# Kernel tuning notes

Measured on AMD Instinct MI355X. Metric: run time of the kernel, lower is better.

Reference implementation:

```python
import jax, jax.numpy as jnp
import numpy as np
from jax import lax

V, E, H, B, S = 100000, 256, 256, 16, 64
NEG = -1e9


def setup_inputs() -> dict:
    key = jax.random.key(0)
    ks = jax.random.split(key, 20)
    sc = 0.05
    inp = {
        "x": jax.random.randint(ks[0], (B, S), 0, V),
        "mask": jax.random.randint(ks[1], (B, S), 0, 2).astype(jnp.int32),
        "TASK": 0,
        # embedding table (pretrained embedding copied into nn.Embedding)
        "embed": jax.random.normal(ks[2], (V, E), jnp.float32) * sc,
        # shared LSTM (torch gate order i,f,g,o)
        "W_ih": jax.random.normal(ks[3], (4 * H, E), jnp.float32) * sc,
        "W_hh": jax.random.normal(ks[4], (4 * H, H), jnp.float32) * sc,
        "b_ih": jax.random.normal(ks[5], (4 * H,), jnp.float32) * sc,
        "b_hh": jax.random.normal(ks[6], (4 * H,), jnp.float32) * sc,
        # task-specific attention: Ws: (E+2H)->H, Us: H->1
        "Ws_w": jax.random.normal(ks[7], (H, E + 2 * H), jnp.float32) * sc,
        "Ws_b": jax.random.normal(ks[8], (H,), jnp.float32) * sc,
        "Us_w": jax.random.normal(ks[9], (1, H), jnp.float32) * sc,
        "Us_b": jax.random.normal(ks[10], (1,), jnp.float32) * sc,
        # message LSTM cell: gates from x_t, h_{t-1}, message Rt
        "Wx": jax.random.normal(ks[11], (4 * H, E), jnp.float32) * sc,
        "Wh": jax.random.normal(ks[12], (4 * H, H), jnp.float32) * sc,
        "Wm": jax.random.normal(ks[13], (4 * H, H), jnp.float32) * sc,
        "b_cell": jax.random.normal(ks[14], (4 * H,), jnp.float32) * sc,
        # final classifier
        "fc_w": jax.random.normal(ks[15], (1, H), jnp.float32) * sc,
        "fc_b": jax.random.normal(ks[16], (1,), jnp.float32) * sc,
    }
    return inp


def _lstm_gates(g, c):
    i, f, gg, o = jnp.split(g, 4, axis=-1)
    c_new = jax.nn.sigmoid(f) * c + jax.nn.sigmoid(i) * jnp.tanh(gg)
    h_new = jax.nn.sigmoid(o) * jnp.tanh(c_new)
    return h_new, c_new


def _forward(x, mask, embed, W_ih, W_hh, b_ih, b_hh, Ws_w, Ws_b, Us_w, Us_b,
             Wx, Wh, Wm, b_cell, fc_w, fc_b):
    b, s = x.shape
    h_dim = W_hh.shape[1]
    emb = embed[x]                              # [B,S,E]
    emb_t = jnp.transpose(emb, (1, 0, 2))       # [S,B,E]
    z = jnp.zeros((b, h_dim), emb.dtype)

    def shared_step(carry, e_t):
        h, c = carry
        g = e_t @ W_ih.T + h @ W_hh.T + (b_ih + b_hh)
        h, c = _lstm_gates(g, c)
        return (h, c), h

    _, shared_t = lax.scan(shared_step, (z, z), emb_t)   # [S,B,H]
    shared = jnp.transpose(shared_t, (1, 0, 2))          # [B,S,H]
    valid = mask != 0                                    # [B,S]

    def task_step(carry, e_t):
        h, c = carry
        h_task = jnp.broadcast_to(h[:, None, :], shared.shape)      # [B,S,H]
        cat = jnp.concatenate([shared, h_task, emb], axis=2)        # [B,S,E+2H]
        var2 = jnp.tanh(cat @ Ws_w.T + Ws_b)                        # [B,S,H]
        Si = (var2 @ Us_w.T + Us_b)[..., 0]                         # [B,S]
        att = jax.nn.softmax(jnp.where(valid, Si, NEG), axis=1)     # masked softmax over S
        Rt = jnp.einsum('bs,bsh->bh', att, shared)                  # [B,H]
        g = e_t @ Wx.T + h @ Wh.T + Rt @ Wm.T + b_cell
        h, c = _lstm_gates(g, c)
        return (h, c), None

    (h_last, _), _ = lax.scan(jax.checkpoint(task_step), (z, z), emb_t)
    return jax.nn.sigmoid(h_last @ fc_w.T + fc_b)        # [B,1]


def reference(x, mask, TASK, embed, W_ih, W_hh, b_ih, b_hh, Ws_w, Ws_b,
              Us_w, Us_b, Wx, Wh, Wm, b_cell, fc_w, fc_b):
    # TASK selects an entry of task_specific_lstm_list, but the list holds the
    # same module object num_tasks times, so one parameter set is used.
    del TASK
    return _forward(x, mask, embed, W_ih, W_hh, b_ih, b_hh, Ws_w, Ws_b,
                    Us_w, Us_b, Wx, Wh, Wm, b_cell, fc_w, fc_b)
```

## Files before the change

### kernel.cpp

```cpp
#include <hip/hip_runtime.h>

#define NEGV -1e9f

#define OFF_X1   0u
#define OFF_XX   1048576u
#define OFF_A    2097152u
#define OFF_SH   2359296u
#define OFF_SWM  2621440u
#define OFF_HX2  3670016u
#define OFF_HX4  3686400u
#define OFF_PSI  3702784u
#define OFF_AT   OFF_X1

__device__ __forceinline__ float sigf(float x) { return 1.f / (1.f + __expf(-x)); }
__device__ __forceinline__ float tanhfast(float x) {
  float e = __expf(2.f * x);
  return 1.f - __fdividef(2.f, e + 1.f);
}

__device__ __forceinline__ unsigned long long gloadU64(const unsigned long long* p) {
  return __hip_atomic_load(p, __ATOMIC_RELAXED, __HIP_MEMORY_SCOPE_AGENT);
}
__device__ __forceinline__ void gstoreU64(unsigned long long* p, unsigned long long v) {
  __hip_atomic_store(p, v, __ATOMIC_RELAXED, __HIP_MEMORY_SCOPE_AGENT);
}

__device__ __forceinline__ void tile_mm(const float* __restrict__ W, int ldw, int wcol0,
                                        int j0, const float* eL, float* wL, float acc[8]) {
  const int i = threadIdx.x >> 4, jj = threadIdx.x & 15;
  for (int kc = 0; kc < 4; ++kc) {
    __syncthreads();
    const int k0 = kc * 64;
    #pragma unroll
    for (int m = 0; m < 32; ++m) {
      int v = threadIdx.x + (m << 8);
      int row = v >> 6, col = v & 63;
      wL[row * 68 + col] = W[(j0 + row) * ldw + wcol0 + k0 + col];
    }
    __syncthreads();
    const float* ebase = eL + i * 260 + k0;
    #pragma unroll 4
    for (int k4 = 0; k4 < 16; ++k4) {
      float4 e4 = *(const float4*)(ebase + k4 * 4);
      #pragma unroll
      for (int u = 0; u < 8; ++u) {
        float4 w4 = *(const float4*)(wL + (jj + (u << 4)) * 68 + k4 * 4);
        acc[u] += e4.x * w4.x + e4.y * w4.y + e4.z * w4.z + e4.w * w4.w;
      }
    }
  }
}

__global__ __launch_bounds__(256) void k1_precompute(
    const int* __restrict__ x, const float* __restrict__ embed,
    const float* __restrict__ W_ih, const float* __restrict__ b_ih,
    const float* __restrict__ b_hh, const float* __restrict__ Ws_w,
    const float* __restrict__ Ws_b, const float* __restrict__ Wx,
    const float* __restrict__ b_cell, float* __restrict__ ws) {
  __shared__ float eL[16 * 260];
  __shared__ float wL[128 * 68];
  const int rt = blockIdx.x / 18, jb = blockIdx.x % 18;
  if (blockIdx.x == 0) {
    for (int i = threadIdx.x; i < 65536; i += 256) ws[OFF_HX2 + i] = 0.f;
  }
  for (int i = 0; i < 16; ++i) {
    int xi = x[rt * 16 + i];
    eL[i * 260 + threadIdx.x] = embed[xi * 256 + threadIdx.x];
  }
  const float* W; const float* bias1; const float* bias2 = nullptr;
  int ldw, wcol0, j0, ostride; float* out;
  if (jb < 8)       { W = W_ih; ldw = 256; wcol0 = 0;   j0 = jb * 128;        out = ws + OFF_X1; ostride = 1024; bias1 = b_ih; bias2 = b_hh; }
  else if (jb < 16) { W = Wx;   ldw = 256; wcol0 = 0;   j0 = (jb - 8) * 128;  out = ws + OFF_XX; ostride = 1024; bias1 = b_cell; }
  else              { W = Ws_w; ldw = 768; wcol0 = 512; j0 = (jb - 16) * 128; out = ws + OFF_A;  ostride = 256;  bias1 = Ws_b; }
  float acc[8];
  #pragma unroll
  for (int u = 0; u < 8; ++u) acc[u] = 0.f;
  tile_mm(W, ldw, wcol0, j0, eL, wL, acc);
  const int i = threadIdx.x >> 4, jj = threadIdx.x & 15;
  const int r = rt * 16 + i;
  #pragma unroll
  for (int u = 0; u < 8; ++u) {
    int j = j0 + jj + (u << 4);
    float bv = bias1[j] + (bias2 ? bias2[j] : 0.f);
    out[r * ostride + j] = acc[u] + bv;
  }
}

__global__ __launch_bounds__(512) void k2_shared_lstm(
    const float* __restrict__ W_hh, float* __restrict__ ws) {
  const int b = blockIdx.x & 15, j = blockIdx.x >> 4;
  const int t = threadIdx.x;
  const int rl = t >> 2, q = t & 3;
  const int grow = ((rl >> 5) << 8) + (j << 5) + (rl & 31);
  __shared__ float x1L[64 * 128];
  __shared__ __align__(16) float hL[256];
  __shared__ float gA[128];
  unsigned long long* hx = (unsigned long long*)(ws + OFF_HX2);
  float* sh = ws + OFF_SH;
  const float* X1 = ws + OFF_X1;

  float4 wv[16];
  {
    const float* wp = W_hh + grow * 256 + (q << 6);
    #pragma unroll
    for (int m = 0; m < 16; ++m) wv[m] = *(const float4*)(wp + 4 * m);
  }
  for (int v = t; v < 8192; v += 512) {
    int st = v >> 7, r = v & 127;
    int col = ((r >> 5) << 8) + (j << 5) + (r & 31);
    x1L[v] = X1[(b * 64 + st) * 1024 + col];
  }
  float c_reg = 0.f;
  __syncthreads();

  for (int st = 0; st < 64; ++st) {
    if (t < 256) {
      const unsigned long long* p = hx + (unsigned)(st & 1) * 4096u + b * 256 + t;
      unsigned long long v = gloadU64(p);
      while ((unsigned)(v >> 32) < (unsigned)st) v = gloadU64(p);
      hL[t] = __uint_as_float((unsigned)v);
    }
    __syncthreads();
    float p = 0.f;
    const float* hp = hL + (q << 6);
    #pragma unroll
    for (int m = 0; m < 16; ++m) {
      float4 h4 = *(const float4*)(hp + 4 * m);
      p += wv[m].x * h4.x + wv[m].y * h4.y + wv[m].z * h4.z + wv[m].w * h4.w;
    }
    p += __shfl_xor(p, 1); p += __shfl_xor(p, 2);
    if (q == 0) gA[rl] = p + x1L[st * 128 + rl];
    __syncthreads();
    if (t < 32) {
      float gi = gA[t], gf = gA[32 + t], gg = gA[64 + t], go = gA[96 + t];
      c_reg = sigf(gf) * c_reg + sigf(gi) * tanhfast(gg);
      float hn = sigf(go) * tanhfast(c_reg);
      sh[(b * 64 + st) * 256 + (j << 5) + t] = hn;
      unsigned long long pv = ((unsigned long long)(unsigned)(st + 1) << 32)
                            | (unsigned long long)__float_as_uint(hn);
      gstoreU64(hx + (unsigned)((st + 1) & 1) * 4096u + b * 256 + (j << 5) + t, pv);
    }
  }
}

__global__ __launch_bounds__(256) void k3_precompute2(
    const float* __restrict__ Ws_w, const float* __restrict__ Wm,
    float* __restrict__ ws) {
  __shared__ float eL[16 * 260];
  __shared__ float wL[128 * 68];
  const int rt = blockIdx.x / 10, jb = blockIdx.x % 10;
  const float* sh = ws + OFF_SH;
  for (int i = 0; i < 16; ++i)
    eL[i * 260 + threadIdx.x] = sh[(rt * 16 + i) * 256 + threadIdx.x];
  const float* W; int ldw, wcol0, j0; bool addmode;
  if (jb < 8) { W = Wm;   ldw = 256; wcol0 = 0; j0 = jb * 128;       addmode = false; }
  else        { W = Ws_w; ldw = 768; wcol0 = 0; j0 = (jb - 8) * 128; addmode = true; }
  float acc[8];
  #pragma unroll
  for (int u = 0; u < 8; ++u) acc[u] = 0.f;
  tile_mm(W, ldw, wcol0, j0, eL, wL, acc);
  const int i = threadIdx.x >> 4, jj = threadIdx.x & 15;
  const int r = rt * 16 + i;
  if (addmode) {
    const float* Aemb = ws + OFF_A;
    float* AT = ws + OFF_AT;
    const int bb = r >> 6, s = r & 63;
    #pragma unroll
    for (int u = 0; u < 8; ++u) {
      int j = j0 + jj + (u << 4);
      AT[bb * 16384 + j * 64 + s] = Aemb[r * 256 + j] + acc[u];
    }
  } else {
    float* out = ws + OFF_SWM;
    #pragma unroll
    for (int u = 0; u < 8; ++u) {
      int j = j0 + jj + (u << 4);
      out[r * 1024 + j] = acc[u];
    }
  }
}

__global__ __launch_bounds__(512) void k4_task_lstm(
    const int* __restrict__ mask, const float* __restrict__ Ws_w,
    const float* __restrict__ Us_w, const float* __restrict__ Wh,
    const float* __restrict__ fc_w, const float* __restrict__ fc_b,
    float* __restrict__ ws, float* __restrict__ out) {
  const int b = blockIdx.x & 15, j = blockIdx.x >> 4;
  const int t = threadIdx.x;
  const int rl = t >> 2, q = t & 3;
  const int grow = ((rl >> 5) << 8) + (j << 5) + (rl & 31);
  const int hwrow = t >> 4, hwc = t & 15;
  const int kq = t >> 6, sl = t & 63;

  __shared__ __align__(16) float swmB[4 * 128 * 20];
  __shared__ __align__(16) float aTo[32 * 65];
  __shared__ __align__(16) float hL[256];
  __shared__ float hwOwn[32];
  __shared__ float usOwn[32];
  __shared__ float part[8 * 64];
  __shared__ float psiA[512];
  __shared__ __align__(16) float attL[64];
  __shared__ float gA[128];
  __shared__ float redL[4];
  __shared__ int   mL[64];

  unsigned long long* hx   = (unsigned long long*)(ws + OFF_HX4);
  unsigned long long* psiX = (unsigned long long*)(ws + OFF_PSI);
  const float* AT  = ws + OFF_AT;
  const float* SWM = ws + OFF_SWM;
  const float* Xx  = ws + OFF_XX;

  float4 w2v[4];
  {
    const float* p2 = Ws_w + (j * 32 + hwrow) * 768 + 256 + (hwc << 4);
    #pragma unroll
    for (int m = 0; m < 4; ++m) w2v[m] = *(const float4*)(p2 + 4 * m);
  }
  float4 whv[16];
  {
    const float* pw = Wh + grow * 256 + (q << 6);
    #pragma unroll
    for (int m = 0; m < 16; ++m) whv[m] = *(const float4*)(pw + 4 * m);
  }
  for (int v = t; v < 2048; v += 512)
    aTo[(v >> 6) * 65 + (v & 63)] = AT[b * 16384 + j * 2048 + v];
  for (int v = t; v < 8192; v += 512) {
    int s = v >> 7, r = v & 127;
    int col = ((r >> 5) << 8) + (j << 5) + (r & 31);
    swmB[(s >> 4) * 2560 + r * 20 + (s & 15)] = SWM[(b * 64 + s) * 1024 + col];
  }
  if (t < 32) usOwn[t] = Us_w[j * 32 + t];
  if (t < 64) mL[t] = mask[b * 64 + t];
  float c_reg = 0.f;
  __syncthreads();

  for (int st = 0; st < 64; ++st) {
    float xx_r = 0.f;
    if (q == 0) xx_r = Xx[(b * 64 + st) * 1024 + grow];
    if (t < 256) {
      const unsigned long long* p = hx + (unsigned)(st & 1) * 4096u + b * 256 + t;
      unsigned long long v = gloadU64(p);
      while ((unsigned)(v >> 32) < (unsigned)st) v = gloadU64(p);
      hL[t] = __uint_as_float((unsigned)v);
    }
    __syncthreads();
    {
      const float* hp = hL + (hwc << 4);
      float p = 0.f;
      #pragma unroll
      for (int m = 0; m < 4; ++m) {
        float4 h4 = *(const float4*)(hp + 4 * m);
        p += w2v[m].x * h4.x + w2v[m].y * h4.y + w2v[m].z * h4.z + w2v[m].w * h4.w;
      }
      p += __shfl_xor(p, 1); p += __shfl_xor(p, 2);
      p += __shfl_xor(p, 4); p += __shfl_xor(p, 8);
      if (hwc == 0) hwOwn[hwrow] = p;
    }
    __syncthreads();
    {
      float ps = 0.f;
      #pragma unroll
      for (int i2 = 0; i2 < 4; ++i2) {
        int kk = (kq << 2) + i2;
        ps += usOwn[kk] * tanhfast(aTo[kk * 65 + sl] + hwOwn[kk]);
      }
      part[(kq << 6) + sl] = ps;
    }
    __syncthreads();
    if (t < 64) {
      float ps = 0.f;
      #pragma unroll
      for (int w = 0; w < 8; ++w) ps += part[(w << 6) + t];
      unsigned long long pv = ((unsigned long long)(unsigned)(st + 1) << 32)
                            | (unsigned long long)__float_as_uint(ps);
      gstoreU64(psiX + ((unsigned)(st & 1) * 16u + b) * 512u + (j << 6) + t, pv);
    }
    float pwh = 0.f;
    {
      const float* hp = hL + (q << 6);
      #pragma unroll
      for (int m = 0; m < 16; ++m) {
        float4 h4 = *(const float4*)(hp + 4 * m);
        pwh += whv[m].x * h4.x + whv[m].y * h4.y + whv[m].z * h4.z + whv[m].w * h4.w;
      }
    }
    {
      const unsigned long long* p = psiX + ((unsigned)(st & 1) * 16u + b) * 512u + t;
      unsigned long long v = gloadU64(p);
      while ((unsigned)(v >> 32) < (unsigned)(st + 1)) v = gloadU64(p);
      psiA[t] = __uint_as_float((unsigned)v);
    }
    __syncthreads();
    if (t < 64) {
      float acc = 0.f;
      #pragma unroll
      for (int w = 0; w < 8; ++w) acc += psiA[(w << 6) + t];
      float v = mL[t] ? acc : NEGV;
      float mx = v;
      #pragma unroll
      for (int d = 1; d < 64; d <<= 1) mx = fmaxf(mx, __shfl_xor(mx, d));
      float e = __expf(v - mx);
      float ssum = e;
      #pragma unroll
      for (int d = 1; d < 64; d <<= 1) ssum += __shfl_xor(ssum, d);
      attL[t] = e / ssum;
    }
    __syncthreads();
    {
      float p = pwh;
      const float* sb = swmB + q * 2560 + rl * 20;
      const float* atb = attL + (q << 4);
      #pragma unroll
      for (int i2 = 0; i2 < 4; ++i2) {
        float4 s4 = *(const float4*)(sb + 4 * i2);
        float4 a4 = *(const float4*)(atb + 4 * i2);
        p += s4.x * a4.x + s4.y * a4.y + s4.z * a4.z + s4.w * a4.w;
      }
      p += __shfl_xor(p, 1); p += __shfl_xor(p, 2);
      if (q == 0) gA[rl] = p + xx_r;
    }
    __syncthreads();
    if (t < 32) {
      float gi = gA[t], gf = gA[32 + t], gg = gA[64 + t], go = gA[96 + t];
      c_reg = sigf(gf) * c_reg + sigf(gi) * tanhfast(gg);
      float hn = sigf(go) * tanhfast(c_reg);
      unsigned long long pv = ((unsigned long long)(unsigned)(st + 1) << 32)
                            | (unsigned long long)__float_as_uint(hn);
      gstoreU64(hx + (unsigned)((st + 1) & 1) * 4096u + b * 256 + (j << 5) + t, pv);
    }
  }

  if (j == 0) {
    float v = 0.f;
    if (t < 256) {
      const unsigned long long* p = hx + 0 * 4096u + b * 256 + t;
      unsigned long long vv = gloadU64(p);
      while ((unsigned)(vv >> 32) < 64u) vv = gloadU64(p);
      v = __uint_as_float((unsigned)vv) * fc_w[t];
    }
    #pragma unroll
    for (int d = 1; d < 64; d <<= 1) v += __shfl_xor(v, d);
    if (t < 256 && (t & 63) == 0) redL[t >> 6] = v;
    __syncthreads();
    if (t == 0) out[b] = sigf(redL[0] + redL[1] + redL[2] + redL[3] + fc_b[0]);
  }
}

extern "C" void kernel_launch(void* const* d_in, const int* in_sizes, int n_in,
                              void* d_out, int out_size, void* d_ws, size_t ws_size,
                              hipStream_t stream) {
  const int*   x      = (const int*)d_in[0];
  const int*   mask   = (const int*)d_in[1];
  const float* embed  = (const float*)d_in[3];
  const float* W_ih   = (const float*)d_in[4];
  const float* W_hh   = (const float*)d_in[5];
  const float* b_ih   = (const float*)d_in[6];
  const float* b_hh   = (const float*)d_in[7];
  const float* Ws_w   = (const float*)d_in[8];
  const float* Ws_b   = (const float*)d_in[9];
  const float* Us_w   = (const float*)d_in[10];
  const float* Wx     = (const float*)d_in[12];
  const float* Wh     = (const float*)d_in[13];
  const float* Wm     = (const float*)d_in[14];
  const float* b_cell = (const float*)d_in[15];
  const float* fc_w   = (const float*)d_in[16];
  const float* fc_b   = (const float*)d_in[17];
  float* ws  = (float*)d_ws;
  float* out = (float*)d_out;

  k1_precompute<<<dim3(1152), dim3(256), 0, stream>>>(
      x, embed, W_ih, b_ih, b_hh, Ws_w, Ws_b, Wx, b_cell, ws);
  k2_shared_lstm<<<dim3(128), dim3(512), 0, stream>>>(W_hh, ws);
  k3_precompute2<<<dim3(640), dim3(256), 0, stream>>>(Ws_w, Wm, ws);
  k4_task_lstm<<<dim3(128), dim3(512), 0, stream>>>(
      mask, Ws_w, Us_w, Wh, fc_w, fc_b, ws, out);
}
```

Baseline: 436.4 us.

## Fuse shared LSTM, second precompute and task LSTM into one persistent kernel

Merges the shared-LSTM recurrence, the shared-state projections (Ws_w and Wm applied to the shared hidden states) and the task LSTM into one 128-block kernel. Per-batch release/acquire flags replace the kernel boundaries. Each block now computes its own slice of the attention pre-activations and Wm products from a transposed shared-state tile in LDS. This removes two launches and the global round trip of the SWM and AT intermediates. In exchange the 640-block GEMM becomes per-block FMA work on only 128 blocks, and LDS use per block grows considerably.

```diff
diff --git a/kernel.cpp b/kernel.cpp
--- a/kernel.cpp
+++ b/kernel.cpp
@@ -6,11 +6,10 @@
 #define OFF_XX   1048576u
 #define OFF_A    2097152u
 #define OFF_SH   2359296u
-#define OFF_SWM  2621440u
 #define OFF_HX2  3670016u
 #define OFF_HX4  3686400u
 #define OFF_PSI  3702784u
-#define OFF_AT   OFF_X1
+#define OFF_FLG  3735552u
 
 __device__ __forceinline__ float sigf(float x) { return 1.f / (1.f + __expf(-x)); }
 __device__ __forceinline__ float tanhfast(float x) {
@@ -23,6 +22,21 @@
 }
 __device__ __forceinline__ void gstoreU64(unsigned long long* p, unsigned long long v) {
   __hip_atomic_store(p, v, __ATOMIC_RELAXED, __HIP_MEMORY_SCOPE_AGENT);
+}
+__device__ __forceinline__ float gloadF(const float* p) {
+  return __hip_atomic_load(p, __ATOMIC_RELAXED, __HIP_MEMORY_SCOPE_AGENT);
+}
+__device__ __forceinline__ void gstoreF(float* p, float v) {
+  __hip_atomic_store(p, v, __ATOMIC_RELAXED, __HIP_MEMORY_SCOPE_AGENT);
+}
+__device__ __forceinline__ unsigned gloadAcq(const unsigned* p) {
+  return __hip_atomic_load(p, __ATOMIC_ACQUIRE, __HIP_MEMORY_SCOPE_AGENT);
+}
+__device__ __forceinline__ void gstoreRel(unsigned* p, unsigned v) {
+  __hip_atomic_store(p, v, __ATOMIC_RELEASE, __HIP_MEMORY_SCOPE_AGENT);
+}
+__device__ __forceinline__ unsigned long long packTV(unsigned tag, float v) {
+  return ((unsigned long long)tag << 32) | (unsigned long long)__float_as_uint(v);
 }
 
 __device__ __forceinline__ void tile_mm(const float* __restrict__ W, int ldw, int wcol0,
@@ -61,7 +75,7 @@
   __shared__ float wL[128 * 68];
   const int rt = blockIdx.x / 18, jb = blockIdx.x % 18;
   if (blockIdx.x == 0) {
-    for (int i = threadIdx.x; i < 65536; i += 256) ws[OFF_HX2 + i] = 0.f;
+    for (int i = threadIdx.x; i < 65792; i += 256) ws[OFF_HX2 + i] = 0.f;
   }
   for (int i = 0; i < 16; ++i) {
     int xi = x[rt * 16 + i];
@@ -86,263 +100,252 @@
   }
 }
 
-__global__ __launch_bounds__(512) void k2_shared_lstm(
-    const float* __restrict__ W_hh, float* __restrict__ ws) {
-  const int b = blockIdx.x & 15, j = blockIdx.x >> 4;
-  const int t = threadIdx.x;
-  const int rl = t >> 2, q = t & 3;
-  const int grow = ((rl >> 5) << 8) + (j << 5) + (rl & 31);
-  __shared__ float x1L[64 * 128];
-  __shared__ __align__(16) float hL[256];
-  __shared__ float gA[128];
-  unsigned long long* hx = (unsigned long long*)(ws + OFF_HX2);
-  float* sh = ws + OFF_SH;
-  const float* X1 = ws + OFF_X1;
-
-  float4 wv[16];
-  {
-    const float* wp = W_hh + grow * 256 + (q << 6);
-    #pragma unroll
-    for (int m = 0; m < 16; ++m) wv[m] = *(const float4*)(wp + 4 * m);
-  }
-  for (int v = t; v < 8192; v += 512) {
-    int st = v >> 7, r = v & 127;
-    int col = ((r >> 5) << 8) + (j << 5) + (r & 31);
-    x1L[v] = X1[(b * 64 + st) * 1024 + col];
-  }
-  float c_reg = 0.f;
-  __syncthreads();
-
-  for (int st = 0; st < 64; ++st) {
-    if (t < 256) {
-      const unsigned long long* p = hx + (unsigned)(st & 1) * 4096u + b * 256 + t;
-      unsigned long long v = gloadU64(p);
-      while ((unsigned)(v >> 32) < (unsigned)st) v = gloadU64(p);
-      hL[t] = __uint_as_float((unsigned)v);
-    }
-    __syncthreads();
-    float p = 0.f;
-    const float* hp = hL + (q << 6);
-    #pragma unroll
-    for (int m = 0; m < 16; ++m) {
-      float4 h4 = *(const float4*)(hp + 4 * m);
-      p += wv[m].x * h4.x + wv[m].y * h4.y + wv[m].z * h4.z + wv[m].w * h4.w;
-    }
-    p += __shfl_xor(p, 1); p += __shfl_xor(p, 2);
-    if (q == 0) gA[rl] = p + x1L[st * 128 + rl];
-    __syncthreads();
-    if (t < 32) {
-      float gi = gA[t], gf = gA[32 + t], gg = gA[64 + t], go = gA[96 + t];
-      c_reg = sigf(gf) * c_reg + sigf(gi) * tanhfast(gg);
-      float hn = sigf(go) * tanhfast(c_reg);
-      sh[(b * 64 + st) * 256 + (j << 5) + t] = hn;
-      unsigned long long pv = ((unsigned long long)(unsigned)(st + 1) << 32)
-                            | (unsigned long long)__float_as_uint(hn);
-      gstoreU64(hx + (unsigned)((st + 1) & 1) * 4096u + b * 256 + (j << 5) + t, pv);
-    }
-  }
-}
-
-__global__ __launch_bounds__(256) void k3_precompute2(
-    const float* __restrict__ Ws_w, const float* __restrict__ Wm,
-    float* __restrict__ ws) {
-  __shared__ float eL[16 * 260];
-  __shared__ float wL[128 * 68];
-  const int rt = blockIdx.x / 10, jb = blockIdx.x % 10;
-  const float* sh = ws + OFF_SH;
-  for (int i = 0; i < 16; ++i)
-    eL[i * 260 + threadIdx.x] = sh[(rt * 16 + i) * 256 + threadIdx.x];
-  const float* W; int ldw, wcol0, j0; bool addmode;
-  if (jb < 8) { W = Wm;   ldw = 256; wcol0 = 0; j0 = jb * 128;       addmode = false; }
-  else        { W = Ws_w; ldw = 768; wcol0 = 0; j0 = (jb - 8) * 128; addmode = true; }
-  float acc[8];
-  #pragma unroll
-  for (int u = 0; u < 8; ++u) acc[u] = 0.f;
-  tile_mm(W, ldw, wcol0, j0, eL, wL, acc);
-  const int i = threadIdx.x >> 4, jj = threadIdx.x & 15;
-  const int r = rt * 16 + i;
-  if (addmode) {
-    const float* Aemb = ws + OFF_A;
-    float* AT = ws + OFF_AT;
-    const int bb = r >> 6, s = r & 63;
-    #pragma unroll
-    for (int u = 0; u < 8; ++u) {
-      int j = j0 + jj + (u << 4);
-      AT[bb * 16384 + j * 64 + s] = Aemb[r * 256 + j] + acc[u];
-    }
-  } else {
-    float* out = ws + OFF_SWM;
-    #pragma unroll
-    for (int u = 0; u < 8; ++u) {
-      int j = j0 + jj + (u << 4);
-      out[r * 1024 + j] = acc[u];
-    }
-  }
-}
-
-__global__ __launch_bounds__(512) void k4_task_lstm(
-    const int* __restrict__ mask, const float* __restrict__ Ws_w,
-    const float* __restrict__ Us_w, const float* __restrict__ Wh,
+__global__ __launch_bounds__(512) void k_fused(
+    const int* __restrict__ mask, const float* __restrict__ W_hh,
+    const float* __restrict__ Ws_w, const float* __restrict__ Us_w,
+    const float* __restrict__ Wh, const float* __restrict__ Wm,
     const float* __restrict__ fc_w, const float* __restrict__ fc_b,
     float* __restrict__ ws, float* __restrict__ out) {
   const int b = blockIdx.x & 15, j = blockIdx.x >> 4;
   const int t = threadIdx.x;
-  const int rl = t >> 2, q = t & 3;
-  const int grow = ((rl >> 5) << 8) + (j << 5) + (rl & 31);
-  const int hwrow = t >> 4, hwc = t & 15;
-  const int kq = t >> 6, sl = t & 63;
-
-  __shared__ __align__(16) float swmB[4 * 128 * 20];
+  const int w = t >> 6, l = t & 63;
+
+  __shared__ __align__(16) float bigL[256 * 65];
   __shared__ __align__(16) float aTo[32 * 65];
+  __shared__ __align__(16) float swmB[10240];
   __shared__ __align__(16) float hL[256];
   __shared__ float hwOwn[32];
   __shared__ float usOwn[32];
-  __shared__ float part[8 * 64];
+  __shared__ float part[512];
   __shared__ float psiA[512];
   __shared__ __align__(16) float attL[64];
   __shared__ float gA[128];
   __shared__ float redL[4];
   __shared__ int   mL[64];
 
-  unsigned long long* hx   = (unsigned long long*)(ws + OFF_HX4);
+  float* shg = ws + OFF_SH;
+  const float* X1   = ws + OFF_X1;
+  const float* Xx   = ws + OFF_XX;
+  const float* Aemb = ws + OFF_A;
+  unsigned long long* hx2  = (unsigned long long*)(ws + OFF_HX2);
+  unsigned long long* hx4  = (unsigned long long*)(ws + OFF_HX4);
   unsigned long long* psiX = (unsigned long long*)(ws + OFF_PSI);
-  const float* AT  = ws + OFF_AT;
-  const float* SWM = ws + OFF_SWM;
-  const float* Xx  = ws + OFF_XX;
-
-  float4 w2v[4];
+  unsigned* flg = (unsigned*)(ws + OFF_FLG);
+
   {
-    const float* p2 = Ws_w + (j * 32 + hwrow) * 768 + 256 + (hwc << 4);
-    #pragma unroll
-    for (int m = 0; m < 4; ++m) w2v[m] = *(const float4*)(p2 + 4 * m);
-  }
-  float4 whv[16];
-  {
-    const float* pw = Wh + grow * 256 + (q << 6);
-    #pragma unroll
-    for (int m = 0; m < 16; ++m) whv[m] = *(const float4*)(pw + 4 * m);
-  }
-  for (int v = t; v < 2048; v += 512)
-    aTo[(v >> 6) * 65 + (v & 63)] = AT[b * 16384 + j * 2048 + v];
-  for (int v = t; v < 8192; v += 512) {
-    int s = v >> 7, r = v & 127;
-    int col = ((r >> 5) << 8) + (j << 5) + (r & 31);
-    swmB[(s >> 4) * 2560 + r * 20 + (s & 15)] = SWM[(b * 64 + s) * 1024 + col];
-  }
-  if (t < 32) usOwn[t] = Us_w[j * 32 + t];
-  if (t < 64) mL[t] = mask[b * 64 + t];
-  float c_reg = 0.f;
-  __syncthreads();
-
-  for (int st = 0; st < 64; ++st) {
-    float xx_r = 0.f;
-    if (q == 0) xx_r = Xx[(b * 64 + st) * 1024 + grow];
-    if (t < 256) {
-      const unsigned long long* p = hx + (unsigned)(st & 1) * 4096u + b * 256 + t;
-      unsigned long long v = gloadU64(p);
-      while ((unsigned)(v >> 32) < (unsigned)st) v = gloadU64(p);
-      hL[t] = __uint_as_float((unsigned)v);
-    }
-    __syncthreads();
+    const int rl = t >> 2, q = t & 3;
+    const int grow = ((rl >> 5) << 8) + (j << 5) + (rl & 31);
+    float4 wv[16];
     {
-      const float* hp = hL + (hwc << 4);
+      const float* wp = W_hh + grow * 256 + (q << 6);
+      #pragma unroll
+      for (int m = 0; m < 16; ++m) wv[m] = *(const float4*)(wp + 4 * m);
+    }
+    for (int v = t; v < 8192; v += 512) {
+      int st = v >> 7, rr = v & 127;
+      int col = ((rr >> 5) << 8) + (j << 5) + (rr & 31);
+      bigL[v] = X1[(b * 64 + st) * 1024 + col];
+    }
+    float c_reg = 0.f;
+    __syncthreads();
+    for (int st = 0; st < 64; ++st) {
+      if (t < 256) {
+        const unsigned long long* p = hx2 + (unsigned)(st & 1) * 4096u + b * 256 + t;
+        unsigned long long v = gloadU64(p);
+        while ((unsigned)(v >> 32) < (unsigned)st) v = gloadU64(p);
+        hL[t] = __uint_as_float((unsigned)v);
+      }
+      __syncthreads();
+      const float* hp = hL + (q << 6);
       float p = 0.f;
-      #pragma unroll
-      for (int m = 0; m < 4; ++m) {
-        float4 h4 = *(const float4*)(hp + 4 * m);
-        p += w2v[m].x * h4.x + w2v[m].y * h4.y + w2v[m].z * h4.z + w2v[m].w * h4.w;
-      }
-      p += __shfl_xor(p, 1); p += __shfl_xor(p, 2);
-      p += __shfl_xor(p, 4); p += __shfl_xor(p, 8);
-      if (hwc == 0) hwOwn[hwrow] = p;
-    }
-    __syncthreads();
-    {
-      float ps = 0.f;
-      #pragma unroll
-      for (int i2 = 0; i2 < 4; ++i2) {
-        int kk = (kq << 2) + i2;
-        ps += usOwn[kk] * tanhfast(aTo[kk * 65 + sl] + hwOwn[kk]);
-      }
-      part[(kq << 6) + sl] = ps;
-    }
-    __syncthreads();
-    if (t < 64) {
-      float ps = 0.f;
-      #pragma unroll
-      for (int w = 0; w < 8; ++w) ps += part[(w << 6) + t];
-      unsigned long long pv = ((unsigned long long)(unsigned)(st + 1) << 32)
-                            | (unsigned long long)__float_as_uint(ps);
-      gstoreU64(psiX + ((unsigned)(st & 1) * 16u + b) * 512u + (j << 6) + t, pv);
-    }
-    float pwh = 0.f;
-    {
-      const float* hp = hL + (q << 6);
       #pragma unroll
       for (int m = 0; m < 16; ++m) {
         float4 h4 = *(const float4*)(hp + 4 * m);
-        pwh += whv[m].x * h4.x + whv[m].y * h4.y + whv[m].z * h4.z + whv[m].w * h4.w;
-      }
-    }
+        p += wv[m].x * h4.x + wv[m].y * h4.y + wv[m].z * h4.z + wv[m].w * h4.w;
+      }
+      p += __shfl_xor(p, 1); p += __shfl_xor(p, 2);
+      if (q == 0) gA[rl] = p + bigL[(st << 7) + rl];
+      __syncthreads();
+      if (t < 32) {
+        float gi = gA[t], gf = gA[32 + t], gg = gA[64 + t], go = gA[96 + t];
+        c_reg = sigf(gf) * c_reg + sigf(gi) * tanhfast(gg);
+        float hn = sigf(go) * tanhfast(c_reg);
+        gstoreF(shg + (b * 64 + st) * 256 + (j << 5) + t, hn);
+        gstoreU64(hx2 + (unsigned)((st + 1) & 1) * 4096u + b * 256 + (j << 5) + t,
+                  packTV(st + 1, hn));
+      }
+    }
+    __syncthreads();
+    if (t == 0) gstoreRel(flg + b * 16 + j, 1u);
+  }
+  if (t < 8) { while (gloadAcq(flg + b * 16 + t) < 1u) {} }
+  __syncthreads();
+
+  for (int v = t; v < 16384; v += 512) {
+    int s = v >> 8, m = v & 255;
+    bigL[m * 65 + s] = gloadF(shg + (unsigned)(b * 64 + s) * 256u + m);
+  }
+  __syncthreads();
+  #pragma unroll
+  for (int i2 = 0; i2 < 4; ++i2) {
+    int kk = (w << 2) + i2;
+    int gk = (j << 5) + kk;
+    const float* wr = Ws_w + gk * 768;
+    float acc = 0.f;
+    #pragma unroll 4
+    for (int m = 0; m < 256; m += 4) {
+      float4 w4 = *(const float4*)(wr + m);
+      acc += w4.x * bigL[m * 65 + l]       + w4.y * bigL[(m + 1) * 65 + l]
+           + w4.z * bigL[(m + 2) * 65 + l] + w4.w * bigL[(m + 3) * 65 + l];
+    }
+    aTo[kk * 65 + l] = acc + Aemb[(b * 64 + l) * 256 + gk];
+  }
+  for (int i2 = 0; i2 < 16; ++i2) {
+    int c = (i2 << 3) + w;
+    int gcol = ((c >> 5) << 8) + (j << 5) + (c & 31);
+    const float* wr = Wm + gcol * 256;
+    float acc = 0.f;
+    #pragma unroll 4
+    for (int m = 0; m < 256; m += 4) {
+      float4 w4 = *(const float4*)(wr + m);
+      acc += w4.x * bigL[m * 65 + l]       + w4.y * bigL[(m + 1) * 65 + l]
+           + w4.z * bigL[(m + 2) * 65 + l] + w4.w * bigL[(m + 3) * 65 + l];
+    }
+    swmB[(l >> 4) * 2560 + c * 20 + (l & 15)] = acc;
+  }
+  __syncthreads();
+
+  {
+    const int rl = t >> 2, q = t & 3;
+    const int grow = ((rl >> 5) << 8) + (j << 5) + (rl & 31);
+    const int hwrow = t >> 4, hwc = t & 15;
+    const int kq = t >> 6, sl = t & 63;
+
+    float4 w2v[4];
     {
-      const unsigned long long* p = psiX + ((unsigned)(st & 1) * 16u + b) * 512u + t;
-      unsigned long long v = gloadU64(p);
-      while ((unsigned)(v >> 32) < (unsigned)(st + 1)) v = gloadU64(p);
-      psiA[t] = __uint_as_float((unsigned)v);
-    }
-    __syncthreads();
-    if (t < 64) {
-      float acc = 0.f;
-      #pragma unroll
-      for (int w = 0; w < 8; ++w) acc += psiA[(w << 6) + t];
-      float v = mL[t] ? acc : NEGV;
-      float mx = v;
-      #pragma unroll
-      for (int d = 1; d < 64; d <<= 1) mx = fmaxf(mx, __shfl_xor(mx, d));
-      float e = __expf(v - mx);
-      float ssum = e;
-      #pragma unroll
-      for (int d = 1; d < 64; d <<= 1) ssum += __shfl_xor(ssum, d);
-      attL[t] = e / ssum;
-    }
-    __syncthreads();
+      const float* p2 = Ws_w + (j * 32 + hwrow) * 768 + 256 + (hwc << 4);
+      #pragma unroll
+      for (int m = 0; m < 4; ++m) w2v[m] = *(const float4*)(p2 + 4 * m);
+    }
+    float4 whv[16];
     {
-      float p = pwh;
-      const float* sb = swmB + q * 2560 + rl * 20;
-      const float* atb = attL + (q << 4);
-      #pragma unroll
-      for (int i2 = 0; i2 < 4; ++i2) {
-        float4 s4 = *(const float4*)(sb + 4 * i2);
-        float4 a4 = *(const float4*)(atb + 4 * i2);
-        p += s4.x * a4.x + s4.y * a4.y + s4.z * a4.z + s4.w * a4.w;
-      }
-      p += __shfl_xor(p, 1); p += __shfl_xor(p, 2);
-      if (q == 0) gA[rl] = p + xx_r;
-    }
-    __syncthreads();
-    if (t < 32) {
-      float gi = gA[t], gf = gA[32 + t], gg = gA[64 + t], go = gA[96 + t];
-      c_reg = sigf(gf) * c_reg + sigf(gi) * tanhfast(gg);
-      float hn = sigf(go) * tanhfast(c_reg);
-      unsigned long long pv = ((unsigned long long)(unsigned)(st + 1) << 32)
-                            | (unsigned long long)__float_as_uint(hn);
-      gstoreU64(hx + (unsigned)((st + 1) & 1) * 4096u + b * 256 + (j << 5) + t, pv);
-    }
-  }
-
-  if (j == 0) {
-    float v = 0.f;
-    if (t < 256) {
-      const unsigned long long* p = hx + 0 * 4096u + b * 256 + t;
-      unsigned long long vv = gloadU64(p);
-      while ((unsigned)(vv >> 32) < 64u) vv = gloadU64(p);
-      v = __uint_as_float((unsigned)vv) * fc_w[t];
-    }
-    #pragma unroll
-    for (int d = 1; d < 64; d <<= 1) v += __shfl_xor(v, d);
-    if (t < 256 && (t & 63) == 0) redL[t >> 6] = v;
-    __syncthreads();
-    if (t == 0) out[b] = sigf(redL[0] + redL[1] + redL[2] + redL[3] + fc_b[0]);
+      const float* pw = Wh + grow * 256 + (q << 6);
+      #pragma unroll
+      for (int m = 0; m < 16; ++m) whv[m] = *(const float4*)(pw + 4 * m);
+    }
+    if (t < 32) usOwn[t] = Us_w[j * 32 + t];
+    if (t < 64) mL[t] = mask[b * 64 + t];
+    float c_reg = 0.f;
+    __syncthreads();
+
+    for (int st = 0; st < 64; ++st) {
+      float xx_r = 0.f;
+      if (q == 0) xx_r = Xx[(b * 64 + st) * 1024 + grow];
+      if (t < 256) {
+        const unsigned long long* p = hx4 + (unsigned)(st & 1) * 4096u + b * 256 + t;
+        unsigned long long v = gloadU64(p);
+        while ((unsigned)(v >> 32) < (unsigned)st) v = gloadU64(p);
+        hL[t] = __uint_as_float((unsigned)v);
+      }
+      __syncthreads();
+      {
+        const float* hp = hL + (hwc << 4);
+        float p = 0.f;
+        #pragma unroll
+        for (int m = 0; m < 4; ++m) {
+          float4 h4 = *(const float4*)(hp + 4 * m);
+          p += w2v[m].x * h4.x + w2v[m].y * h4.y + w2v[m].z * h4.z + w2v[m].w * h4.w;
+        }
+        p += __shfl_xor(p, 1); p += __shfl_xor(p, 2);
+        p += __shfl_xor(p, 4); p += __shfl_xor(p, 8);
+        if (hwc == 0) hwOwn[hwrow] = p;
+      }
+      __syncthreads();
+      {
+        float ps = 0.f;
+        #pragma unroll
+        for (int i2 = 0; i2 < 4; ++i2) {
+          int kk = (kq << 2) + i2;
+          ps += usOwn[kk] * tanhfast(aTo[kk * 65 + sl] + hwOwn[kk]);
+        }
+        part[(kq << 6) + sl] = ps;
+      }
+      __syncthreads();
+      if (t < 64) {
+        float ps = 0.f;
+        #pragma unroll
+        for (int w2 = 0; w2 < 8; ++w2) ps += part[(w2 << 6) + t];
+        gstoreU64(psiX + ((unsigned)(st & 1) * 16u + b) * 512u + (j << 6) + t,
+                  packTV(st + 1, ps));
+      }
+      float pwh = 0.f;
+      {
+        const float* hp = hL + (q << 6);
+        #pragma unroll
+        for (int m = 0; m < 16; ++m) {
+          float4 h4 = *(const float4*)(hp + 4 * m);
+          pwh += whv[m].x * h4.x + whv[m].y * h4.y + whv[m].z * h4.z + whv[m].w * h4.w;
+        }
+      }
+      {
+        const unsigned long long* p = psiX + ((unsigned)(st & 1) * 16u + b) * 512u + t;
+        unsigned long long v = gloadU64(p);
+        while ((unsigned)(v >> 32) < (unsigned)(st + 1)) v = gloadU64(p);
+        psiA[t] = __uint_as_float((unsigned)v);
+      }
+      __syncthreads();
+      if (t < 64) {
+        float acc = 0.f;
+        #pragma unroll
+        for (int w2 = 0; w2 < 8; ++w2) acc += psiA[(w2 << 6) + t];
+        float v = mL[t] ? acc : NEGV;
+        float mx = v;
+        #pragma unroll
+        for (int d = 1; d < 64; d <<= 1) mx = fmaxf(mx, __shfl_xor(mx, d));
+        float e = __expf(v - mx);
+        float ssum = e;
+        #pragma unroll
+        for (int d = 1; d < 64; d <<= 1) ssum += __shfl_xor(ssum, d);
+        attL[t] = e / ssum;
+      }
+      __syncthreads();
+      {
+        float p = pwh;
+        const float* sb = swmB + q * 2560 + rl * 20;
+        const float* atb = attL + (q << 4);
+        #pragma unroll
+        for (int i2 = 0; i2 < 4; ++i2) {
+          float4 s4 = *(const float4*)(sb + 4 * i2);
+          float4 a4 = *(const float4*)(atb + 4 * i2);
+          p += s4.x * a4.x + s4.y * a4.y + s4.z * a4.z + s4.w * a4.w;
+        }
+        p += __shfl_xor(p, 1); p += __shfl_xor(p, 2);
+        if (q == 0) gA[rl] = p + xx_r;
+      }
+      __syncthreads();
+      if (t < 32) {
+        float gi = gA[t], gf = gA[32 + t], gg = gA[64 + t], go = gA[96 + t];
+        c_reg = sigf(gf) * c_reg + sigf(gi) * tanhfast(gg);
+        float hn = sigf(go) * tanhfast(c_reg);
+        gstoreU64(hx4 + (unsigned)((st + 1) & 1) * 4096u + b * 256 + (j << 5) + t,
+                  packTV(st + 1, hn));
+      }
+    }
+
+    if (j == 0) {
+      float v = 0.f;
+      if (t < 256) {
+        const unsigned long long* p = hx4 + 0 * 4096u + b * 256 + t;
+        unsigned long long vv = gloadU64(p);
+        while ((unsigned)(vv >> 32) < 64u) vv = gloadU64(p);
+        v = __uint_as_float((unsigned)vv) * fc_w[t];
+      }
+      #pragma unroll
+      for (int d = 1; d < 64; d <<= 1) v += __shfl_xor(v, d);
+      if (t < 256 && (t & 63) == 0) redL[t >> 6] = v;
+      __syncthreads();
+      if (t == 0) out[b] = sigf(redL[0] + redL[1] + redL[2] + redL[3] + fc_b[0]);
+    }
   }
 }
 
@@ -370,8 +373,6 @@
 
   k1_precompute<<<dim3(1152), dim3(256), 0, stream>>>(
       x, embed, W_ih, b_ih, b_hh, Ws_w, Ws_b, Wx, b_cell, ws);
-  k2_shared_lstm<<<dim3(128), dim3(512), 0, stream>>>(W_hh, ws);
-  k3_precompute2<<<dim3(640), dim3(256), 0, stream>>>(Ws_w, Wm, ws);
-  k4_task_lstm<<<dim3(128), dim3(512), 0, stream>>>(
-      mask, Ws_w, Us_w, Wh, fc_w, fc_b, ws, out);
-}
+  k_fused<<<dim3(128), dim3(512), 0, stream>>>(
+      mask, W_hh, Ws_w, Us_w, Wh, Wm, fc_w, fc_b, ws, out);
+}
```

Measured after the change: 521.5 us. 1.19x slower.
